# Performance work log

Measured on AMD Instinct MI355X. Metric: run time of the kernel, lower is better.

Reference implementation:

```python
import jax, jax.numpy as jnp
import numpy as np

N = 4096   # patients
D = 256    # encoding dim per modality
EPS = 1e-8 # torch CosineSimilarity eps


def setup_inputs() -> dict:
    key = jax.random.key(0)
    ks = jax.random.split(key, 7)
    return {
        "log_hazard": jax.random.normal(ks[0], (N,), dtype=jnp.float32),
        "time": jax.random.randint(ks[1], (N,), 0, 3650, dtype=jnp.int32),
        "event": jax.random.randint(ks[2], (N,), 0, 2, dtype=jnp.int32),
        "eb0": jax.random.normal(ks[3], (N, D), dtype=jnp.float32),
        "eb1": jax.random.normal(ks[4], (N, D), dtype=jnp.float32),
        "eb2": jax.random.normal(ks[5], (N, D), dtype=jnp.float32),
        "eb3": jax.random.normal(ks[6], (N, D), dtype=jnp.float32),
        "M_margin": 1,
    }


def _cox_npll(h, t, e):
    # risk_matrix = (outer(t,t) >= t^2).T  ->  risk[i,j] = (t_j * t_i >= t_i^2)
    tt = t[:, None] * t[None, :]                      # [N,N] = t_i * t_j
    risk = (tt >= (t * t)[:, None]).astype(h.dtype)   # row i: patients j with t_j >= t_i
    log_denom = jnp.log(risk @ jnp.exp(h))            # [N]
    ef = e.astype(h.dtype)
    return -jnp.sum(ef * (h - log_denom)) / jnp.sum(ef)


def _similarity_loss(blocks, margin):
    # Vectorized form of the O(N^2 * n_mod) pairwise loop.
    matched = jnp.zeros((N, N), dtype=blocks[0].dtype)  # sum_mod cos(x_i, x_j) over valid mods
    own = jnp.zeros((N, N), dtype=blocks[0].dtype)      # sum_mod cos(x_i, x_i) over valid mods
    for x in blocks:
        nrm = jnp.linalg.norm(x, axis=1)                # [N]
        den = jnp.maximum(nrm, EPS)
        xn = x / den[:, None]
        S = xn @ xn.T                                   # cos(x_i, x_j) with torch eps semantics
        diag = (nrm * nrm) / (den * den)                # cos(x_i, x_i)
        miss = jnp.all(x == x[:, :1], axis=1)           # modality missing (constant row)
        valid = (~(miss[:, None] | miss[None, :])).astype(x.dtype)
        matched = matched + valid * S
        own = own + valid * diag[:, None]
    offdiag = 1.0 - jnp.eye(N, dtype=matched.dtype)
    per_pair = jax.nn.relu(margin - matched + own)
    return jnp.sum(offdiag * per_pair)


def reference(log_hazard, time, event, eb0, eb1, eb2, eb3, M_margin):
    margin = jnp.float32(M_margin)
    cox = _cox_npll(log_hazard, time, event)
    sim = _similarity_loss([eb0, eb1, eb2, eb3], margin)
    return cox + sim
```

## Files before the change

### kernel.cpp

```cpp
#include <hip/hip_runtime.h>
#include <stdint.h>

#define NPAT 4096
#define DIM  256
#define EPSV 1e-8f
#define BT   128
#define NT   (NPAT / BT)
#define NBLK (NT * (NT + 1) / 2)
#define NSTEP 16
#define NBINS 4096

typedef float f32x4  __attribute__((ext_vector_type(4)));
typedef float f32x16 __attribute__((ext_vector_type(16)));
typedef int   i32x8  __attribute__((ext_vector_type(8)));

#define WS_DVAL_OFF 256
#define WS_MVEC_OFF (WS_DVAL_OFF + 16*NPAT)
#define WS_XN_OFF   (WS_MVEC_OFF + 16*NPAT)

__device__ __forceinline__ float decode_margin(const int* pm) {
  int v = *pm;
  if (v > -16777216 && v < 16777216) return (float)v;
  return __int_as_float(v);
}

__global__ __launch_bounds__(256) void prep_kernel(
    const float4* __restrict__ eb0, const float4* __restrict__ eb1,
    const float4* __restrict__ eb2, const float4* __restrict__ eb3,
    uint8_t* __restrict__ XnF, float* __restrict__ dval_f,
    float* __restrict__ mvec_f, float* __restrict__ scal)
{
  const int i    = blockIdx.x;
  const int wv   = threadIdx.x >> 6;
  const int lane = threadIdx.x & 63;
  const float4* ebs[4] = {eb0, eb1, eb2, eb3};
  const float4 v = ebs[wv][i * (DIM / 4) + lane];
  float s = v.x * v.x + v.y * v.y + v.z * v.z + v.w * v.w;
#pragma unroll
  for (int o = 32; o; o >>= 1) s += __shfl_down(s, o, 64);
  s = __shfl(s, 0, 64);
  const float x0 = __shfl(v.x, 0, 64);
  const bool eq = (v.x == x0) && (v.y == x0) && (v.z == x0) && (v.w == x0);
  const bool miss = (__ballot(eq) == ~0ull);
  const float nrm = sqrtf(s);
  const float den = fmaxf(nrm, EPSV);
  const float inv = miss ? 0.0f : (1.0f / den);
  int p = 0;
  p = __builtin_amdgcn_cvt_pk_fp8_f32(v.x * inv, v.y * inv, p, false);
  p = __builtin_amdgcn_cvt_pk_fp8_f32(v.z * inv, v.w * inv, p, true);
  const int g  = i >> 5, r = i & 31;
  const int ss = wv * 4 + (lane >> 4);
  const int h  = (lane >> 3) & 1;
  const int b  = (lane & 7) * 4;
  *(int*)&XnF[(size_t)((g * 16 + ss) * 64 + (h * 32 + r)) * 32 + b] = p;
  if (lane == 0) {
    const float diag = (nrm * nrm) / (den * den);
    dval_f[i * 4 + wv] = miss ? 0.0f : diag;
    mvec_f[i * 4 + wv] = miss ? 0.0f : 1.0f;
  }
  if (i == 0 && threadIdx.x == 0) {
    scal[0] = 0.0f;
    scal[1] = 0.0f;
    ((unsigned*)scal)[2] = 0u;
  }
}

__global__ __launch_bounds__(256, 3) void sim_gemm_kernel(
    const uint8_t* __restrict__ XnF, const float4* __restrict__ dval,
    const float4* __restrict__ mvec, const int* __restrict__ pmargin,
    const float* __restrict__ h, const int* __restrict__ t,
    const int* __restrict__ e, float* __restrict__ scal,
    float* __restrict__ out)
{
  __shared__ __align__(16) uint8_t smem[16384 + 256];
  const int L   = blockIdx.x;
  const int tid = threadIdx.x;
  const int lane = tid & 63, wvv = tid >> 6;

  if (L == 0) {
    float* bins = (float*)smem;
    float* wt   = (float*)(smem + 16384);
    float* rn   = (float*)(smem + 16384 + 32);
    float* rd   = (float*)(smem + 16384 + 64);
#pragma unroll
    for (int k = 0; k < 16; ++k) bins[tid + k * 256] = 0.0f;
    __syncthreads();
#pragma unroll
    for (int k = 0; k < 16; ++k) {
      const int i = tid + k * 256;
      atomicAdd(&bins[t[i]], expf(h[i]));
    }
    __syncthreads();
    float seg[16]; float part = 0.0f;
#pragma unroll
    for (int k = 0; k < 16; ++k) { seg[k] = bins[tid * 16 + k]; part += seg[k]; }
    float sfx = part;
#pragma unroll
    for (int off = 1; off < 64; off <<= 1) {
      const float u = __shfl_down(sfx, off, 64);
      if (lane + off < 64) sfx += u;
    }
    if (lane == 0) wt[wvv] = sfx;
    __syncthreads();
    float above = 0.0f;
    for (int w = wvv + 1; w < 4; ++w) above += wt[w];
    float run = above + (sfx - part);
#pragma unroll
    for (int k = 15; k >= 0; --k) { run += seg[k]; bins[tid * 16 + k] = run; }
    __syncthreads();
    float nloc = 0.0f, dloc = 0.0f;
#pragma unroll
    for (int k = 0; k < 16; ++k) {
      const int i = tid + k * 256;
      const float ei = (float)e[i];
      if (ei != 0.0f) { nloc += ei * (h[i] - logf(bins[t[i]])); dloc += ei; }
    }
#pragma unroll
    for (int o = 32; o; o >>= 1) {
      nloc += __shfl_down(nloc, o, 64);
      dloc += __shfl_down(dloc, o, 64);
    }
    if (lane == 0) { rn[wvv] = nloc; rd[wvv] = dloc; }
    __syncthreads();
    if (tid == 0) {
      float n = 0.0f, d = 0.0f;
#pragma unroll
      for (int k = 0; k < 4; ++k) { n += rn[k]; d += rd[k]; }
      atomicExch(&scal[1], n / d);
      __threadfence();
      const unsigned old = atomicAdd(&((unsigned*)scal)[2], 1u);
      if (old == NBLK) {
        __threadfence();
        out[0] = atomicAdd(&scal[0], 0.0f) - (n / d);
      }
    }
    return;
  }

  const int T = L - 1;
  int bi = (int)((2 * NT + 1 - sqrtf((float)((2 * NT + 1) * (2 * NT + 1)) - 8.0f * T)) * 0.5f);
  if (bi < 0) bi = 0;
  if (bi > NT - 1) bi = NT - 1;
  while (bi > 0 && bi * NT - bi * (bi - 1) / 2 > T) --bi;
  while ((bi + 1) * NT - (bi + 1) * bi / 2 <= T) ++bi;
  const int bj = bi + (T - (bi * NT - bi * (bi - 1) / 2));

  const int wi = wvv >> 1, wj = wvv & 1;
  const int gA0 = bi * 4 + wi * 2;
  const int gB0 = bj * 4 + wj * 2;
  const uint8_t* pA = XnF + (size_t)(gA0 * 16) * 2048 + lane * 32;
  const uint8_t* pB = XnF + (size_t)(gB0 * 16) * 2048 + lane * 32;

  f32x16 acc[2][2] = {};

#pragma unroll 2
  for (int s = 0; s < NSTEP; ++s) {
    const i32x8 a0 = *(const i32x8*)(pA + (size_t)s * 2048);
    const i32x8 a1 = *(const i32x8*)(pA + 32768 + (size_t)s * 2048);
    const i32x8 b0 = *(const i32x8*)(pB + (size_t)s * 2048);
    const i32x8 b1 = *(const i32x8*)(pB + 32768 + (size_t)s * 2048);
    acc[0][0] = __builtin_amdgcn_mfma_scale_f32_32x32x64_f8f6f4(
        a0, b0, acc[0][0], 0, 0, 0, 0x7F7F7F7F, 0, 0x7F7F7F7F);
    acc[0][1] = __builtin_amdgcn_mfma_scale_f32_32x32x64_f8f6f4(
        a0, b1, acc[0][1], 0, 0, 0, 0x7F7F7F7F, 0, 0x7F7F7F7F);
    acc[1][0] = __builtin_amdgcn_mfma_scale_f32_32x32x64_f8f6f4(
        a1, b0, acc[1][0], 0, 0, 0, 0x7F7F7F7F, 0, 0x7F7F7F7F);
    acc[1][1] = __builtin_amdgcn_mfma_scale_f32_32x32x64_f8f6f4(
        a1, b1, acc[1][1], 0, 0, 0, 0x7F7F7F7F, 0, 0x7F7F7F7F);
  }

  float4* eRDi = (float4*)smem;
  float4* eCMi = (float4*)smem + BT;
  float4* eRDj = (float4*)smem + 2 * BT;
  float4* eCMj = (float4*)smem + 3 * BT;
  float*  wred = (float*)(smem + 8192);
  if (tid < BT) {
    eRDi[tid] = dval[bi * BT + tid];
    eCMi[tid] = mvec[bi * BT + tid];
  } else {
    const int ss = tid - BT;
    eRDj[ss] = dval[bj * BT + ss];
    eCMj[ss] = mvec[bj * BT + ss];
  }
  __syncthreads();

  const float margin = decode_margin(pmargin);
  const bool isDiag = (bi == bj);
  float local = 0.0f;
  const int colA = lane & 31, hsel = lane >> 5;
#pragma unroll
  for (int mi = 0; mi < 2; ++mi) {
#pragma unroll
    for (int mj = 0; mj < 2; ++mj) {
      const int jl = wj * 64 + mj * 32 + colA;
      const float4 cmj = eCMj[jl];
      const float4 rdj = eRDj[jl];
#pragma unroll
      for (int rr = 0; rr < 16; ++rr) {
        const int il = wi * 64 + mi * 32 + (rr & 3) + 8 * (rr >> 2) + 4 * hsel;
        const float4 rdi = eRDi[il];
        const float sv = acc[mi][mj][rr];
        const float own_ij = rdi.x * cmj.x + rdi.y * cmj.y + rdi.z * cmj.z + rdi.w * cmj.w;
        const float v1 = fmaxf(margin - sv + own_ij, 0.0f);
        local += (isDiag && il == jl) ? 0.0f : v1;
        if (!isDiag) {
          const float4 cmi = eCMi[il];
          const float own_ji = rdj.x * cmi.x + rdj.y * cmi.y + rdj.z * cmi.z + rdj.w * cmi.w;
          local += fmaxf(margin - sv + own_ji, 0.0f);
        }
      }
    }
  }
#pragma unroll
  for (int o = 32; o; o >>= 1) local += __shfl_down(local, o, 64);
  if (lane == 0) wred[wvv] = local;
  __syncthreads();
  if (tid == 0) {
    atomicAdd(&scal[0], wred[0] + wred[1] + wred[2] + wred[3]);
    __threadfence();
    const unsigned old = atomicAdd(&((unsigned*)scal)[2], 1u);
    if (old == NBLK) {
      __threadfence();
      out[0] = atomicAdd(&scal[0], 0.0f) - atomicAdd(&scal[1], 0.0f);
    }
  }
}

extern "C" void kernel_launch(void* const* d_in, const int* in_sizes, int n_in,
                              void* d_out, int out_size, void* d_ws, size_t ws_size,
                              hipStream_t stream) {
  const float* h    = (const float*)d_in[0];
  const int*   t    = (const int*)  d_in[1];
  const int*   e    = (const int*)  d_in[2];
  const float4* eb0 = (const float4*)d_in[3];
  const float4* eb1 = (const float4*)d_in[4];
  const float4* eb2 = (const float4*)d_in[5];
  const float4* eb3 = (const float4*)d_in[6];
  const int*   pm   = (const int*)  d_in[7];

  char*    ws   = (char*)d_ws;
  float*   scal = (float*)ws;
  float*   dvf  = (float*)(ws + WS_DVAL_OFF);
  float*   mvf  = (float*)(ws + WS_MVEC_OFF);
  uint8_t* XnF  = (uint8_t*)(ws + WS_XN_OFF);

  prep_kernel<<<NPAT, 256, 0, stream>>>(eb0, eb1, eb2, eb3, XnF, dvf, mvf, scal);
  sim_gemm_kernel<<<NBLK + 1, 256, 0, stream>>>(XnF, (const float4*)dvf, (const float4*)mvf,
                                                pm, h, t, e, scal, (float*)d_out);
}
```

Before: 108.2 us.

## Stage FP8 GEMM operands through double-buffered LDS with async global_load_lds

The fp8 operand layout is split into two 16-byte halves, and the GEMM loop now prefetches the next K-step's A/B tiles into double-buffered shared memory via global_load_lds. Operands are then read from LDS instead of each wave loading directly from global memory. Diagonal tiles load only the A side, and waves that share a tile no longer load it twice. This adds two barriers per step and doubles the LDS footprint, which may lower occupancy below the launch bound of 3 blocks.

```diff
diff --git a/kernel.cpp b/kernel.cpp
--- a/kernel.cpp
+++ b/kernel.cpp
@@ -12,6 +12,7 @@
 
 typedef float f32x4  __attribute__((ext_vector_type(4)));
 typedef float f32x16 __attribute__((ext_vector_type(16)));
+typedef int   i32x4  __attribute__((ext_vector_type(4)));
 typedef int   i32x8  __attribute__((ext_vector_type(8)));
 
 #define WS_DVAL_OFF 256
@@ -22,6 +23,13 @@
   int v = *pm;
   if (v > -16777216 && v < 16777216) return (float)v;
   return __int_as_float(v);
+}
+
+__device__ __forceinline__ i32x8 ld_op(const uint8_t* p) {
+  union { i32x8 w; i32x4 h[2]; } u;
+  u.h[0] = *(const i32x4*)(p);
+  u.h[1] = *(const i32x4*)(p + 1024);
+  return u.w;
 }
 
 __global__ __launch_bounds__(256) void prep_kernel(
@@ -51,8 +59,10 @@
   const int g  = i >> 5, r = i & 31;
   const int ss = wv * 4 + (lane >> 4);
   const int h  = (lane >> 3) & 1;
-  const int b  = (lane & 7) * 4;
-  *(int*)&XnF[(size_t)((g * 16 + ss) * 64 + (h * 32 + r)) * 32 + b] = p;
+  const int q  = (lane >> 2) & 1;
+  const int b16 = (lane & 3) * 4;
+  *(int*)&XnF[(size_t)(g * 16 + ss) * 2048 + q * 1024 +
+              (size_t)(h * 32 + r) * 16 + b16] = p;
   if (lane == 0) {
     const float diag = (nrm * nrm) / (den * den);
     dval_f[i * 4 + wv] = miss ? 0.0f : diag;
@@ -72,7 +82,7 @@
     const int* __restrict__ e, float* __restrict__ scal,
     float* __restrict__ out)
 {
-  __shared__ __align__(16) uint8_t smem[16384 + 256];
+  __shared__ __align__(16) uint8_t smem[32768 + 256];
   const int L   = blockIdx.x;
   const int tid = threadIdx.x;
   const int lane = tid & 63, wvv = tid >> 6;
@@ -146,19 +156,38 @@
   const int bj = bi + (T - (bi * NT - bi * (bi - 1) / 2));
 
   const int wi = wvv >> 1, wj = wvv & 1;
-  const int gA0 = bi * 4 + wi * 2;
-  const int gB0 = bj * 4 + wj * 2;
-  const uint8_t* pA = XnF + (size_t)(gA0 * 16) * 2048 + lane * 32;
-  const uint8_t* pB = XnF + (size_t)(gB0 * 16) * 2048 + lane * 32;
+  const bool isDiag = (bi == bj);
+
+#define STAGE(BUFOFF, S) do {                                                        \
+    if (!isDiag || wvv < 2) {                                                        \
+      _Pragma("unroll")                                                              \
+      for (int t_ = 0; t_ < 4; ++t_) {                                               \
+        const int ii = wvv * 4 + t_;                                                 \
+        const int grp = (ii < 8) ? (bi * 4 + (ii >> 1)) : (bj * 4 + ((ii >> 1) & 3));\
+        const uint8_t* src = XnF + (size_t)(grp * 16 + (S)) * 2048                   \
+                             + (ii & 1) * 1024 + lane * 16;                          \
+        uint8_t* dst = (uint8_t*)smem + (BUFOFF) + ii * 1024;                        \
+        __builtin_amdgcn_global_load_lds(                                            \
+            (const __attribute__((address_space(1))) unsigned int*)src,              \
+            (__attribute__((address_space(3))) unsigned int*)dst, 16, 0, 0);         \
+      }                                                                              \
+    }                                                                                \
+  } while (0)
 
   f32x16 acc[2][2] = {};
 
-#pragma unroll 2
+  STAGE(0, 0);
+  int cur = 0;
+#pragma unroll 1
   for (int s = 0; s < NSTEP; ++s) {
-    const i32x8 a0 = *(const i32x8*)(pA + (size_t)s * 2048);
-    const i32x8 a1 = *(const i32x8*)(pA + 32768 + (size_t)s * 2048);
-    const i32x8 b0 = *(const i32x8*)(pB + (size_t)s * 2048);
-    const i32x8 b1 = *(const i32x8*)(pB + 32768 + (size_t)s * 2048);
+    if (s + 1 < NSTEP) STAGE((cur ^ 1) * 16384, s + 1);
+    __syncthreads();
+    const uint8_t* aB = (const uint8_t*)smem + cur * 16384 + (size_t)lane * 16;
+    const uint8_t* bB = aB + (isDiag ? 0 : 8192);
+    const i32x8 a0 = ld_op(aB + (wi * 2 + 0) * 2048);
+    const i32x8 a1 = ld_op(aB + (wi * 2 + 1) * 2048);
+    const i32x8 b0 = ld_op(bB + (wj * 2 + 0) * 2048);
+    const i32x8 b1 = ld_op(bB + (wj * 2 + 1) * 2048);
     acc[0][0] = __builtin_amdgcn_mfma_scale_f32_32x32x64_f8f6f4(
         a0, b0, acc[0][0], 0, 0, 0, 0x7F7F7F7F, 0, 0x7F7F7F7F);
     acc[0][1] = __builtin_amdgcn_mfma_scale_f32_32x32x64_f8f6f4(
@@ -167,7 +196,10 @@
         a1, b0, acc[1][0], 0, 0, 0, 0x7F7F7F7F, 0, 0x7F7F7F7F);
     acc[1][1] = __builtin_amdgcn_mfma_scale_f32_32x32x64_f8f6f4(
         a1, b1, acc[1][1], 0, 0, 0, 0x7F7F7F7F, 0, 0x7F7F7F7F);
-  }
+    __syncthreads();
+    cur ^= 1;
+  }
+#undef STAGE
 
   float4* eRDi = (float4*)smem;
   float4* eCMi = (float4*)smem + BT;
@@ -185,7 +217,6 @@
   __syncthreads();
 
   const float margin = decode_margin(pmargin);
-  const bool isDiag = (bi == bj);
   float local = 0.0f;
   const int colA = lane & 31, hsel = lane >> 5;
 #pragma unroll
```

Measured after the change: 111.1 us. +2.7%, slower.

## Fuse prep and similarity GEMM into one persistent kernel with grid barrier

Applied to the files above, without the earlier changes.

Merges the normalisation/FP8-pack kernel and the similarity GEMM into a single persistent 512-block kernel. Blocks meet at a flag-based grid barrier, then each wave pulls 64x64 triangular tiles from an atomic work counter, and one block also computes the Cox term. This removes a kernel launch and the tail imbalance of the static triangular grid. In exchange each wave now reads its own A and B tiles with less sharing inside a block. The barrier flags are never reset between calls, so repeated launches risk skipping the barrier and racing on the job counter.

```diff
diff --git a/kernel.cpp b/kernel.cpp
--- a/kernel.cpp
+++ b/kernel.cpp
@@ -4,17 +4,19 @@
 #define NPAT 4096
 #define DIM  256
 #define EPSV 1e-8f
-#define BT   128
-#define NT   (NPAT / BT)
-#define NBLK (NT * (NT + 1) / 2)
+#define NT2   64
+#define NJOB  (NT2 * (NT2 + 1) / 2)
 #define NSTEP 16
-#define NBINS 4096
+#define GRID  512
+#define NWAVE (GRID * 4)
+#define NFIN  (NWAVE + 1)
+#define MAGIC 0x9E3779B9u
 
 typedef float f32x4  __attribute__((ext_vector_type(4)));
 typedef float f32x16 __attribute__((ext_vector_type(16)));
 typedef int   i32x8  __attribute__((ext_vector_type(8)));
 
-#define WS_DVAL_OFF 256
+#define WS_DVAL_OFF 4096
 #define WS_MVEC_OFF (WS_DVAL_OFF + 16*NPAT)
 #define WS_XN_OFF   (WS_MVEC_OFF + 16*NPAT)
 
@@ -24,60 +26,69 @@
   return __int_as_float(v);
 }
 
-__global__ __launch_bounds__(256) void prep_kernel(
+__global__ __launch_bounds__(256, 2) void fused_kernel(
     const float4* __restrict__ eb0, const float4* __restrict__ eb1,
     const float4* __restrict__ eb2, const float4* __restrict__ eb3,
-    uint8_t* __restrict__ XnF, float* __restrict__ dval_f,
-    float* __restrict__ mvec_f, float* __restrict__ scal)
+    const float* __restrict__ h, const int* __restrict__ t,
+    const int* __restrict__ e, const int* __restrict__ pmargin,
+    float* __restrict__ scal, unsigned* __restrict__ flags,
+    float* __restrict__ dval_f, float* __restrict__ mvec_f,
+    uint8_t* __restrict__ XnF, float* __restrict__ out)
 {
-  const int i    = blockIdx.x;
-  const int wv   = threadIdx.x >> 6;
-  const int lane = threadIdx.x & 63;
-  const float4* ebs[4] = {eb0, eb1, eb2, eb3};
-  const float4 v = ebs[wv][i * (DIM / 4) + lane];
-  float s = v.x * v.x + v.y * v.y + v.z * v.z + v.w * v.w;
-#pragma unroll
-  for (int o = 32; o; o >>= 1) s += __shfl_down(s, o, 64);
-  s = __shfl(s, 0, 64);
-  const float x0 = __shfl(v.x, 0, 64);
-  const bool eq = (v.x == x0) && (v.y == x0) && (v.z == x0) && (v.w == x0);
-  const bool miss = (__ballot(eq) == ~0ull);
-  const float nrm = sqrtf(s);
-  const float den = fmaxf(nrm, EPSV);
-  const float inv = miss ? 0.0f : (1.0f / den);
-  int p = 0;
-  p = __builtin_amdgcn_cvt_pk_fp8_f32(v.x * inv, v.y * inv, p, false);
-  p = __builtin_amdgcn_cvt_pk_fp8_f32(v.z * inv, v.w * inv, p, true);
-  const int g  = i >> 5, r = i & 31;
-  const int ss = wv * 4 + (lane >> 4);
-  const int h  = (lane >> 3) & 1;
-  const int b  = (lane & 7) * 4;
-  *(int*)&XnF[(size_t)((g * 16 + ss) * 64 + (h * 32 + r)) * 32 + b] = p;
-  if (lane == 0) {
-    const float diag = (nrm * nrm) / (den * den);
-    dval_f[i * 4 + wv] = miss ? 0.0f : diag;
-    mvec_f[i * 4 + wv] = miss ? 0.0f : 1.0f;
-  }
-  if (i == 0 && threadIdx.x == 0) {
+  __shared__ __align__(16) uint8_t smem[16512];
+  const int L = blockIdx.x;
+  const int tid = threadIdx.x;
+  const int lane = tid & 63, wvv = tid >> 6;
+
+  if (L == 0 && tid == 0) {
     scal[0] = 0.0f;
     scal[1] = 0.0f;
     ((unsigned*)scal)[2] = 0u;
-  }
-}
-
-__global__ __launch_bounds__(256, 3) void sim_gemm_kernel(
-    const uint8_t* __restrict__ XnF, const float4* __restrict__ dval,
-    const float4* __restrict__ mvec, const int* __restrict__ pmargin,
-    const float* __restrict__ h, const int* __restrict__ t,
-    const int* __restrict__ e, float* __restrict__ scal,
-    float* __restrict__ out)
-{
-  __shared__ __align__(16) uint8_t smem[16384 + 256];
-  const int L   = blockIdx.x;
-  const int tid = threadIdx.x;
-  const int lane = tid & 63, wvv = tid >> 6;
-
-  if (L == 0) {
+    ((unsigned*)scal)[3] = 0u;
+  }
+
+  {
+    const float4* ebs[4] = {eb0, eb1, eb2, eb3};
+    const int gw = L * 4 + wvv;
+#pragma unroll
+    for (int k = 0; k < 8; ++k) {
+      const int job = gw * 8 + k;
+      const int i = job >> 2, wv = job & 3;
+      const float4 v = ebs[wv][i * (DIM / 4) + lane];
+      float s = v.x * v.x + v.y * v.y + v.z * v.z + v.w * v.w;
+#pragma unroll
+      for (int o = 32; o; o >>= 1) s += __shfl_down(s, o, 64);
+      s = __shfl(s, 0, 64);
+      const float x0 = __shfl(v.x, 0, 64);
+      const bool eq = (v.x == x0) && (v.y == x0) && (v.z == x0) && (v.w == x0);
+      const bool miss = (__ballot(eq) == ~0ull);
+      const float nrm = sqrtf(s);
+      const float den = fmaxf(nrm, EPSV);
+      const float inv = miss ? 0.0f : (1.0f / den);
+      int p = 0;
+      p = __builtin_amdgcn_cvt_pk_fp8_f32(v.x * inv, v.y * inv, p, false);
+      p = __builtin_amdgcn_cvt_pk_fp8_f32(v.z * inv, v.w * inv, p, true);
+      const int g  = i >> 5, r = i & 31;
+      const int ss = wv * 4 + (lane >> 4);
+      const int hh = (lane >> 3) & 1;
+      const int b  = (lane & 7) * 4;
+      *(int*)&XnF[(size_t)((g * 16 + ss) * 64 + (hh * 32 + r)) * 32 + b] = p;
+      if (lane == 0) {
+        const float diag = (nrm * nrm) / (den * den);
+        dval_f[i * 4 + wv] = miss ? 0.0f : diag;
+        mvec_f[i * 4 + wv] = miss ? 0.0f : 1.0f;
+      }
+    }
+  }
+  __syncthreads();
+  if (tid == 0) { __threadfence(); atomicExch(&flags[L], MAGIC); }
+
+  while (atomicAdd(&flags[tid], 0u) != MAGIC) __builtin_amdgcn_s_sleep(2);
+  while (atomicAdd(&flags[tid + 256], 0u) != MAGIC) __builtin_amdgcn_s_sleep(2);
+  __syncthreads();
+  __threadfence();
+
+  if (L == 511) {
     float* bins = (float*)smem;
     float* wt   = (float*)(smem + 16384);
     float* rn   = (float*)(smem + 16384 + 32);
@@ -128,98 +139,98 @@
       for (int k = 0; k < 4; ++k) { n += rn[k]; d += rd[k]; }
       atomicExch(&scal[1], n / d);
       __threadfence();
-      const unsigned old = atomicAdd(&((unsigned*)scal)[2], 1u);
-      if (old == NBLK) {
+      const unsigned old = atomicAdd(&((unsigned*)scal)[3], 1u);
+      if (old == NFIN - 1) {
         __threadfence();
         out[0] = atomicAdd(&scal[0], 0.0f) - (n / d);
       }
     }
-    return;
-  }
-
-  const int T = L - 1;
-  int bi = (int)((2 * NT + 1 - sqrtf((float)((2 * NT + 1) * (2 * NT + 1)) - 8.0f * T)) * 0.5f);
-  if (bi < 0) bi = 0;
-  if (bi > NT - 1) bi = NT - 1;
-  while (bi > 0 && bi * NT - bi * (bi - 1) / 2 > T) --bi;
-  while ((bi + 1) * NT - (bi + 1) * bi / 2 <= T) ++bi;
-  const int bj = bi + (T - (bi * NT - bi * (bi - 1) / 2));
-
-  const int wi = wvv >> 1, wj = wvv & 1;
-  const int gA0 = bi * 4 + wi * 2;
-  const int gB0 = bj * 4 + wj * 2;
-  const uint8_t* pA = XnF + (size_t)(gA0 * 16) * 2048 + lane * 32;
-  const uint8_t* pB = XnF + (size_t)(gB0 * 16) * 2048 + lane * 32;
-
-  f32x16 acc[2][2] = {};
-
+    __syncthreads();
+  }
+
+  const float4* dval = (const float4*)dval_f;
+  const float4* mvec = (const float4*)mvec_f;
+  uint8_t* slice = (uint8_t*)smem + wvv * 4096;
+  float4* eRDi = (float4*)slice;
+  float4* eCMi = (float4*)(slice + 1024);
+  float4* eRDj = (float4*)(slice + 2048);
+  float4* eCMj = (float4*)(slice + 3072);
+  const float margin = decode_margin(pmargin);
+  const int colA = lane & 31, hsel = lane >> 5;
+  float wacc = 0.0f;
+
+  for (;;) {
+    int j = 0;
+    if (lane == 0) j = (int)atomicAdd(&((unsigned*)scal)[2], 1u);
+    j = __shfl(j, 0, 64);
+    if (j >= NJOB) break;
+
+    int bi = (int)((129.0f - sqrtf(129.0f * 129.0f - 8.0f * (float)j)) * 0.5f);
+    if (bi < 0) bi = 0;
+    if (bi > NT2 - 1) bi = NT2 - 1;
+    while (bi > 0 && bi * NT2 - bi * (bi - 1) / 2 > j) --bi;
+    while ((bi + 1) * NT2 - (bi + 1) * bi / 2 <= j) ++bi;
+    const int bj = bi + (j - (bi * NT2 - bi * (bi - 1) / 2));
+    const bool isDiag = (bi == bj);
+
+    const uint8_t* pA = XnF + (size_t)(bi * 2 * 16) * 2048 + (size_t)lane * 32;
+    const uint8_t* pB = XnF + (size_t)(bj * 2 * 16) * 2048 + (size_t)lane * 32;
+    f32x16 acc[2][2] = {};
 #pragma unroll 2
-  for (int s = 0; s < NSTEP; ++s) {
-    const i32x8 a0 = *(const i32x8*)(pA + (size_t)s * 2048);
-    const i32x8 a1 = *(const i32x8*)(pA + 32768 + (size_t)s * 2048);
-    const i32x8 b0 = *(const i32x8*)(pB + (size_t)s * 2048);
-    const i32x8 b1 = *(const i32x8*)(pB + 32768 + (size_t)s * 2048);
-    acc[0][0] = __builtin_amdgcn_mfma_scale_f32_32x32x64_f8f6f4(
-        a0, b0, acc[0][0], 0, 0, 0, 0x7F7F7F7F, 0, 0x7F7F7F7F);
-    acc[0][1] = __builtin_amdgcn_mfma_scale_f32_32x32x64_f8f6f4(
-        a0, b1, acc[0][1], 0, 0, 0, 0x7F7F7F7F, 0, 0x7F7F7F7F);
-    acc[1][0] = __builtin_amdgcn_mfma_scale_f32_32x32x64_f8f6f4(
-        a1, b0, acc[1][0], 0, 0, 0, 0x7F7F7F7F, 0, 0x7F7F7F7F);
-    acc[1][1] = __builtin_amdgcn_mfma_scale_f32_32x32x64_f8f6f4(
-        a1, b1, acc[1][1], 0, 0, 0, 0x7F7F7F7F, 0, 0x7F7F7F7F);
-  }
-
-  float4* eRDi = (float4*)smem;
-  float4* eCMi = (float4*)smem + BT;
-  float4* eRDj = (float4*)smem + 2 * BT;
-  float4* eCMj = (float4*)smem + 3 * BT;
-  float*  wred = (float*)(smem + 8192);
-  if (tid < BT) {
-    eRDi[tid] = dval[bi * BT + tid];
-    eCMi[tid] = mvec[bi * BT + tid];
-  } else {
-    const int ss = tid - BT;
-    eRDj[ss] = dval[bj * BT + ss];
-    eCMj[ss] = mvec[bj * BT + ss];
-  }
-  __syncthreads();
-
-  const float margin = decode_margin(pmargin);
-  const bool isDiag = (bi == bj);
-  float local = 0.0f;
-  const int colA = lane & 31, hsel = lane >> 5;
-#pragma unroll
-  for (int mi = 0; mi < 2; ++mi) {
-#pragma unroll
-    for (int mj = 0; mj < 2; ++mj) {
-      const int jl = wj * 64 + mj * 32 + colA;
-      const float4 cmj = eCMj[jl];
-      const float4 rdj = eRDj[jl];
-#pragma unroll
-      for (int rr = 0; rr < 16; ++rr) {
-        const int il = wi * 64 + mi * 32 + (rr & 3) + 8 * (rr >> 2) + 4 * hsel;
-        const float4 rdi = eRDi[il];
-        const float sv = acc[mi][mj][rr];
-        const float own_ij = rdi.x * cmj.x + rdi.y * cmj.y + rdi.z * cmj.z + rdi.w * cmj.w;
-        const float v1 = fmaxf(margin - sv + own_ij, 0.0f);
-        local += (isDiag && il == jl) ? 0.0f : v1;
-        if (!isDiag) {
-          const float4 cmi = eCMi[il];
-          const float own_ji = rdj.x * cmi.x + rdj.y * cmi.y + rdj.z * cmi.z + rdj.w * cmi.w;
-          local += fmaxf(margin - sv + own_ji, 0.0f);
+    for (int s = 0; s < NSTEP; ++s) {
+      const i32x8 a0 = *(const i32x8*)(pA + (size_t)s * 2048);
+      const i32x8 a1 = *(const i32x8*)(pA + 32768 + (size_t)s * 2048);
+      const i32x8 b0 = *(const i32x8*)(pB + (size_t)s * 2048);
+      const i32x8 b1 = *(const i32x8*)(pB + 32768 + (size_t)s * 2048);
+      acc[0][0] = __builtin_amdgcn_mfma_scale_f32_32x32x64_f8f6f4(
+          a0, b0, acc[0][0], 0, 0, 0, 0x7F7F7F7F, 0, 0x7F7F7F7F);
+      acc[0][1] = __builtin_amdgcn_mfma_scale_f32_32x32x64_f8f6f4(
+          a0, b1, acc[0][1], 0, 0, 0, 0x7F7F7F7F, 0, 0x7F7F7F7F);
+      acc[1][0] = __builtin_amdgcn_mfma_scale_f32_32x32x64_f8f6f4(
+          a1, b0, acc[1][0], 0, 0, 0, 0x7F7F7F7F, 0, 0x7F7F7F7F);
+      acc[1][1] = __builtin_amdgcn_mfma_scale_f32_32x32x64_f8f6f4(
+          a1, b1, acc[1][1], 0, 0, 0, 0x7F7F7F7F, 0, 0x7F7F7F7F);
+    }
+
+    eRDi[lane] = dval[bi * 64 + lane];
+    eCMi[lane] = mvec[bi * 64 + lane];
+    eRDj[lane] = dval[bj * 64 + lane];
+    eCMj[lane] = mvec[bj * 64 + lane];
+
+    float local = 0.0f;
+#pragma unroll
+    for (int mi = 0; mi < 2; ++mi) {
+#pragma unroll
+      for (int mj = 0; mj < 2; ++mj) {
+        const int jl = mj * 32 + colA;
+        const float4 cmj = eCMj[jl];
+        const float4 rdj = eRDj[jl];
+#pragma unroll
+        for (int rr = 0; rr < 16; ++rr) {
+          const int il = mi * 32 + (rr & 3) + 8 * (rr >> 2) + 4 * hsel;
+          const float4 rdi = eRDi[il];
+          const float sv = acc[mi][mj][rr];
+          const float own_ij = rdi.x * cmj.x + rdi.y * cmj.y + rdi.z * cmj.z + rdi.w * cmj.w;
+          const float v1 = fmaxf(margin - sv + own_ij, 0.0f);
+          local += (isDiag && il == jl) ? 0.0f : v1;
+          if (!isDiag) {
+            const float4 cmi = eCMi[il];
+            const float own_ji = rdj.x * cmi.x + rdj.y * cmi.y + rdj.z * cmi.z + rdj.w * cmi.w;
+            local += fmaxf(margin - sv + own_ji, 0.0f);
+          }
         }
       }
     }
-  }
-#pragma unroll
-  for (int o = 32; o; o >>= 1) local += __shfl_down(local, o, 64);
-  if (lane == 0) wred[wvv] = local;
-  __syncthreads();
-  if (tid == 0) {
-    atomicAdd(&scal[0], wred[0] + wred[1] + wred[2] + wred[3]);
+#pragma unroll
+    for (int o = 32; o; o >>= 1) local += __shfl_down(local, o, 64);
+    if (lane == 0) wacc += local;
+  }
+
+  if (lane == 0) {
+    atomicAdd(&scal[0], wacc);
     __threadfence();
-    const unsigned old = atomicAdd(&((unsigned*)scal)[2], 1u);
-    if (old == NBLK) {
+    const unsigned old = atomicAdd(&((unsigned*)scal)[3], 1u);
+    if (old == NFIN - 1) {
       __threadfence();
       out[0] = atomicAdd(&scal[0], 0.0f) - atomicAdd(&scal[1], 0.0f);
     }
@@ -238,13 +249,13 @@
   const float4* eb3 = (const float4*)d_in[6];
   const int*   pm   = (const int*)  d_in[7];
 
-  char*    ws   = (char*)d_ws;
-  float*   scal = (float*)ws;
-  float*   dvf  = (float*)(ws + WS_DVAL_OFF);
-  float*   mvf  = (float*)(ws + WS_MVEC_OFF);
-  uint8_t* XnF  = (uint8_t*)(ws + WS_XN_OFF);
-
-  prep_kernel<<<NPAT, 256, 0, stream>>>(eb0, eb1, eb2, eb3, XnF, dvf, mvf, scal);
-  sim_gemm_kernel<<<NBLK + 1, 256, 0, stream>>>(XnF, (const float4*)dvf, (const float4*)mvf,
-                                                pm, h, t, e, scal, (float*)d_out);
+  char*     ws    = (char*)d_ws;
+  float*    scal  = (float*)ws;
+  unsigned* flags = (unsigned*)(ws + 1024);
+  float*    dvf   = (float*)(ws + WS_DVAL_OFF);
+  float*    mvf   = (float*)(ws + WS_MVEC_OFF);
+  uint8_t*  XnF   = (uint8_t*)(ws + WS_XN_OFF);
+
+  fused_kernel<<<GRID, 256, 0, stream>>>(eb0, eb1, eb2, eb3, h, t, e, pm,
+                                         scal, flags, dvf, mvf, XnF, (float*)d_out);
 }
```

Result: slower. 243.1 us (+124.6%).
